# Performance work log

Hardware: AMD Instinct MI355X
Metric: run time of the kernel (lower is better)

## Reference

```python
import jax, jax.numpy as jnp
import numpy as np


def _gen_grid(flow):
    # flow: [N, 2, H, W] -> grid [N, H, W, 2] in normalized [-1,1] coords
    N, _, H, W = flow.shape
    step_y = 2.0 / H
    step_x = 2.0 / W
    gy = jnp.arange(H, dtype=flow.dtype) * step_y + (-1.0 + 0.5 * step_y)
    gx = jnp.arange(W, dtype=flow.dtype) * step_x + (-1.0 + 0.5 * step_x)
    fp = jnp.transpose(flow, (0, 2, 3, 1))  # [N,H,W,2]
    fx = gx[None, None, :] + fp[..., 0]
    fy = gy[None, :, None] + fp[..., 1]
    fx = jnp.remainder(fx + 1.0, 2.0) - 1.0  # wrap x
    return jnp.stack([fx, fy], axis=-1)


def _grid_sample_bilinear(img, grid):
    # img: [N,C,H,W]; grid: [N,H,W,2] normalized, align_corners=False, zero padding
    N, C, H, W = img.shape
    ihwc = jnp.transpose(img, (0, 2, 3, 1))  # [N,H,W,C]
    x = (grid[..., 0] + 1.0) * (W * 0.5) - 0.5
    y = (grid[..., 1] + 1.0) * (H * 0.5) - 0.5
    x0 = jnp.floor(x)
    y0 = jnp.floor(y)
    tx = x - x0
    ty = y - y0
    x0i = x0.astype(jnp.int32)
    y0i = y0.astype(jnp.int32)
    n = jnp.arange(N)[:, None, None]

    def gather(yi, xi):
        valid = (xi >= 0) & (xi < W) & (yi >= 0) & (yi < H)
        v = ihwc[n, jnp.clip(yi, 0, H - 1), jnp.clip(xi, 0, W - 1)]  # [N,H,W,C]
        return v * valid[..., None].astype(img.dtype)

    out = (gather(y0i, x0i) * ((1 - tx) * (1 - ty))[..., None]
           + gather(y0i, x0i + 1) * (tx * (1 - ty))[..., None]
           + gather(y0i + 1, x0i) * ((1 - tx) * ty)[..., None]
           + gather(y0i + 1, x0i + 1) * (tx * ty)[..., None])
    return jnp.transpose(out, (0, 3, 1, 2))  # [N,C,H,W]


def _compose(flow_prev, img_prev, flow_curr, img_curr):
    grid = _gen_grid(flow_curr)
    return (flow_curr + _grid_sample_bilinear(flow_prev, grid),
            img_curr + _grid_sample_bilinear(img_prev, grid))


def setup_inputs() -> dict:
    key = jax.random.key(0)
    k1, k2 = jax.random.split(key)
    B, L, C, H, W = 4, 32, 32, 128, 128
    flows = jax.random.normal(k1, (B, L, 2, H, W), dtype=jnp.float32) * 0.05
    images = jax.random.normal(k2, (B, L, C, H, W), dtype=jnp.float32)
    return {"flows": flows, "images": images}


def reference(flows, images):
    B, L, _, H, W = flows.shape
    C = images.shape[2]
    cf, ci = flows, images
    step = 1
    while step < L:  # static log2(L) iterations
        Lp = L - step
        pf = cf[:, :-step].reshape(B * Lp, 2, H, W)
        pi = ci[:, :-step].reshape(B * Lp, C, H, W)
        qf = cf[:, step:].reshape(B * Lp, 2, H, W)
        qi = ci[:, step:].reshape(B * Lp, C, H, W)
        nf, ni = _compose(pf, pi, qf, qi)
        cf = jnp.concatenate([cf[:, :step], nf.reshape(B, Lp, 2, H, W)], axis=1)
        ci = jnp.concatenate([ci[:, :step], ni.reshape(B, Lp, C, H, W)], axis=1)
        step *= 2
    return ci
```

## Files before the change

kernel.cpp:

```cpp
#include <hip/hip_runtime.h>


constexpr int B_ = 4, L_ = 32, C_ = 32, H_ = 128, W_ = 128;
constexpr int HW = H_ * W_;
constexpr size_t SLICE_I = (size_t)C_ * HW;
constexpr size_t SLICE_F = (size_t)2  * HW;

typedef unsigned short ush;
typedef unsigned int uint;

__device__ __forceinline__ float uasf(uint u){ union{uint i;float f;}v; v.i=u; return v.f; }
__device__ __forceinline__ uint fasu(float f){ union{float f;uint i;}v; v.f=f; return v.i; }
__device__ __forceinline__ uint f2b_u(float f){ uint i=fasu(f); return (i + 0x7FFFu + ((i>>16)&1u))>>16; }

__device__ __forceinline__ void unpack8(const uint4 u, float* f){
    f[0]=uasf(u.x<<16); f[1]=uasf(u.x&0xFFFF0000u);
    f[2]=uasf(u.y<<16); f[3]=uasf(u.y&0xFFFF0000u);
    f[4]=uasf(u.z<<16); f[5]=uasf(u.z&0xFFFF0000u);
    f[6]=uasf(u.w<<16); f[7]=uasf(u.w&0xFFFF0000u);
}
__device__ __forceinline__ uint4 pack8(const float* f){
    uint4 u;
    u.x = f2b_u(f[0]) | (f2b_u(f[1])<<16);
    u.y = f2b_u(f[2]) | (f2b_u(f[3])<<16);
    u.z = f2b_u(f[4]) | (f2b_u(f[5])<<16);
    u.w = f2b_u(f[6]) | (f2b_u(f[7])<<16);
    return u;
}

__device__ __forceinline__ int swz8(int bid, int chunk) {
    return (bid & 7) * chunk + (bid >> 3);
}

struct Samp { float wm00, wm10, wm01, wm11; int q00, q10, q01, q11; };

__device__ __forceinline__ Samp mk(const float2 fc, const int w, const int h)
{
#pragma clang fp contract(off)
    const float step_x = 2.0f / (float)W_;
    const float step_y = 2.0f / (float)H_;
    const float gx = (float)w * step_x + (-1.0f + 0.5f * step_x);
    const float gy = (float)h * step_y + (-1.0f + 0.5f * step_y);
    float fx = gx + fc.x;
    const float fy = gy + fc.y;
    {
        const float tt = fx + 1.0f;
        float r = fmodf(tt, 2.0f);
        if (r < 0.0f) r += 2.0f;
        fx = r - 1.0f;
    }
    const float x = (fx + 1.0f) * ((float)W_ * 0.5f) - 0.5f;
    const float y = (fy + 1.0f) * ((float)H_ * 0.5f) - 0.5f;
    const float x0f = floorf(x), y0f = floorf(y);
    const float tx = x - x0f, ty = y - y0f;
    const int x0 = (int)x0f, y0 = (int)y0f, x1 = x0 + 1, y1 = y0 + 1;
    const float w00 = (1.0f - tx) * (1.0f - ty);
    const float w10 = tx * (1.0f - ty);
    const float w01 = (1.0f - tx) * ty;
    const float w11 = tx * ty;
    const bool vx0 = (x0 >= 0) & (x0 < W_), vx1 = (x1 >= 0) & (x1 < W_);
    const bool vy0 = (y0 >= 0) & (y0 < H_), vy1 = (y1 >= 0) & (y1 < H_);
    const int xc0 = x0 < 0 ? 0 : (x0 >= W_ ? W_ - 1 : x0);
    const int xc1 = x1 < 0 ? 0 : (x1 >= W_ ? W_ - 1 : x1);
    const int yc0 = y0 < 0 ? 0 : (y0 >= H_ ? H_ - 1 : y0);
    const int yc1 = y1 < 0 ? 0 : (y1 >= H_ ? H_ - 1 : y1);
    Samp s;
    s.wm00 = (vy0 & vx0) ? w00 : 0.0f;
    s.wm10 = (vy0 & vx1) ? w10 : 0.0f;
    s.wm01 = (vy1 & vx0) ? w01 : 0.0f;
    s.wm11 = (vy1 & vx1) ? w11 : 0.0f;
    s.q00 = yc0 * W_ + xc0; s.q10 = yc0 * W_ + xc1;
    s.q01 = yc1 * W_ + xc0; s.q11 = yc1 * W_ + xc1;
    return s;
}

__device__ __forceinline__ float2 flowSamp(const float* __restrict__ pF,
                                           const Samp s, const float2 fc)
{
#pragma clang fp contract(off)
    const float2 a = *(const float2*)(pF + (size_t)s.q00 * 2);
    const float2 b = *(const float2*)(pF + (size_t)s.q10 * 2);
    const float2 c = *(const float2*)(pF + (size_t)s.q01 * 2);
    const float2 d = *(const float2*)(pF + (size_t)s.q11 * 2);
    const float sx = ((a.x * s.wm00 + b.x * s.wm10) + c.x * s.wm01) + d.x * s.wm11;
    const float sy = ((a.y * s.wm00 + b.y * s.wm10) + c.y * s.wm01) + d.y * s.wm11;
    return make_float2(fc.x + sx, fc.y + sy);
}

__global__ __launch_bounds__(256)
void prepass_img(const float* __restrict__ src, ush* __restrict__ P,
                 ush* __restrict__ S, float* __restrict__ outN)
{
    constexpr int NB = 32 * 256;
    const int bid = swz8(blockIdx.x, NB / 8);
    const int wc2 = bid & 1, h = (bid >> 1) & 127, l = bid >> 8;
    __shared__ float lds[32][66];
    const int t = threadIdx.x;
    {
        const int c = t >> 3, wq = t & 7;
        const size_t base = (size_t)l * SLICE_I + (size_t)c * HW + h * W_ + wc2 * 64 + wq * 4;
        const float4 v0 = *(const float4*)(src + base);
        const float4 v1 = *(const float4*)(src + base + 32);
        if (l == 0) {
            *(float4*)(outN + base) = v0;
            *(float4*)(outN + base + 32) = v1;
        }
        lds[c][wq*4+0] = v0.x; lds[c][wq*4+1] = v0.y;
        lds[c][wq*4+2] = v0.z; lds[c][wq*4+3] = v0.w;
        lds[c][wq*4+32] = v1.x; lds[c][wq*4+33] = v1.y;
        lds[c][wq*4+34] = v1.z; lds[c][wq*4+35] = v1.w;
    }
    __syncthreads();
    {
        const int pg = t >> 2, lane4 = t & 3;
        float f[8];
        #pragma unroll
        for (int j = 0; j < 8; ++j) f[j] = lds[lane4*8+j][pg];
        ush* dst = (l == 0) ? S : P;
        *(uint4*)(dst + ((size_t)l * HW + h * W_ + wc2 * 64 + pg) * C_ + lane4 * 8) = pack8(f);
    }
}

__global__ __launch_bounds__(256)
void prepass_flow(const float* __restrict__ src, float* __restrict__ F0,
                  float* __restrict__ SF)
{
    constexpr int NB = 32 * HW / 256;
    const int i = swz8(blockIdx.x, NB / 8) * 256 + threadIdx.x;
    const int l = i >> 14;
    const int p = i & (HW - 1);
    const float f0 = src[(size_t)l * SLICE_F + p];
    const float f1 = src[(size_t)l * SLICE_F + HW + p];
    float* dst = (l == 0) ? SF : F0;
    *(float2*)(dst + (size_t)l * SLICE_F + (size_t)p * 2) = make_float2(f0, f1);
}

template<int STEP>
__global__ __launch_bounds__(256)
void compose(const float* __restrict__ Fcur, const ush* __restrict__ Icur,
             float* __restrict__ Fpong, ush* __restrict__ Ipong,
             ush* __restrict__ S, float* __restrict__ SF,
             float* __restrict__ outN)
{
#pragma clang fp contract(off)
    constexpr int NB = (32 - STEP) * 128;
    const int bid = swz8(blockIdx.x, NB / 8);
    const int wc2 = bid & 1, h2 = (bid >> 1) & 63, l = STEP + (bid >> 7);
    const int t = threadIdx.x, lane4 = t & 3, pg = t >> 2;
    const int w = wc2 * 64 + pg;
    const int hA = 2 * h2, hB = hA + 1;
    const int pA = hA * W_ + w, pB = pA + W_;
    const size_t sI = (size_t)l * SLICE_I;
    const size_t sF = (size_t)l * SLICE_F;

    const int prev = l - STEP;
    const ush*   pI = (prev < STEP) ? (S  + (size_t)prev * SLICE_I)
                                    : (Icur + (size_t)prev * SLICE_I);
    const float* pF = (prev < STEP) ? (SF + (size_t)prev * SLICE_F)
                                    : (Fcur + (size_t)prev * SLICE_F);

    const float2 fcA = *(const float2*)(Fcur + sF + (size_t)pA * 2);
    const float2 fcB = *(const float2*)(Fcur + sF + (size_t)pB * 2);
    const Samp sa = mk(fcA, w, hA);
    const Samp sb = mk(fcB, w, hB);

    const uint4 A00 = *(const uint4*)(pI + (size_t)sa.q00 * C_ + lane4 * 8);
    const uint4 A10 = *(const uint4*)(pI + (size_t)sa.q10 * C_ + lane4 * 8);
    const uint4 A01 = *(const uint4*)(pI + (size_t)sa.q01 * C_ + lane4 * 8);
    const uint4 A11 = *(const uint4*)(pI + (size_t)sa.q11 * C_ + lane4 * 8);
    const uint4 B00 = *(const uint4*)(pI + (size_t)sb.q00 * C_ + lane4 * 8);
    const uint4 B10 = *(const uint4*)(pI + (size_t)sb.q10 * C_ + lane4 * 8);
    const uint4 B01 = *(const uint4*)(pI + (size_t)sb.q01 * C_ + lane4 * 8);
    const uint4 B11 = *(const uint4*)(pI + (size_t)sb.q11 * C_ + lane4 * 8);
    const uint4 CA  = *(const uint4*)(Icur + sI + (size_t)pA * C_ + lane4 * 8);
    const uint4 CB  = *(const uint4*)(Icur + sI + (size_t)pB * C_ + lane4 * 8);

    float oA[8], oB[8];
    {
        float g0[8], g1[8], g2[8], g3[8], cu[8];
        unpack8(A00, g0); unpack8(A10, g1); unpack8(A01, g2); unpack8(A11, g3);
        unpack8(CA, cu);
        #pragma unroll
        for (int j = 0; j < 8; ++j) {
            const float s_ = ((g0[j]*sa.wm00 + g1[j]*sa.wm10) + g2[j]*sa.wm01) + g3[j]*sa.wm11;
            oA[j] = cu[j] + s_;
        }
        unpack8(B00, g0); unpack8(B10, g1); unpack8(B01, g2); unpack8(B11, g3);
        unpack8(CB, cu);
        #pragma unroll
        for (int j = 0; j < 8; ++j) {
            const float s_ = ((g0[j]*sb.wm00 + g1[j]*sb.wm10) + g2[j]*sb.wm01) + g3[j]*sb.wm11;
            oB[j] = cu[j] + s_;
        }
    }

    float2 foA, foB;
    const bool doFlow = (lane4 == 0) && (STEP < 16);
    if (doFlow) {
        foA = flowSamp(pF, sa, fcA);
        foB = flowSamp(pF, sb, fcB);
    }

    __shared__ float lds[32][66];
    const bool fin = (STEP == 16) || (l < 2 * STEP);
    if (fin) {
        #pragma unroll
        for (int j = 0; j < 8; ++j) lds[lane4*8+j][pg] = oA[j];
        __syncthreads();
        {
            const int c = t >> 3, wq = t & 7;
            float v[8];
            #pragma unroll
            for (int j2 = 0; j2 < 4; ++j2) {
                const float2 e = *(const float2*)&lds[c][wq*8 + 2*j2];
                v[2*j2] = e.x; v[2*j2+1] = e.y;
            }
            float* dst = outN + sI + (size_t)c * HW + hA * W_ + wc2 * 64 + wq * 8;
            *(float4*)dst       = make_float4(v[0], v[1], v[2], v[3]);
            *(float4*)(dst + 4) = make_float4(v[4], v[5], v[6], v[7]);
        }
        __syncthreads();
        #pragma unroll
        for (int j = 0; j < 8; ++j) lds[lane4*8+j][pg] = oB[j];
        __syncthreads();
        {
            const int c = t >> 3, wq = t & 7;
            float v[8];
            #pragma unroll
            for (int j2 = 0; j2 < 4; ++j2) {
                const float2 e = *(const float2*)&lds[c][wq*8 + 2*j2];
                v[2*j2] = e.x; v[2*j2+1] = e.y;
            }
            float* dst = outN + sI + (size_t)c * HW + hB * W_ + wc2 * 64 + wq * 8;
            *(float4*)dst       = make_float4(v[0], v[1], v[2], v[3]);
            *(float4*)(dst + 4) = make_float4(v[4], v[5], v[6], v[7]);
        }
        if constexpr (STEP < 16) {
            *(uint4*)(S + sI + (size_t)pA * C_ + lane4 * 8) = pack8(oA);
            *(uint4*)(S + sI + (size_t)pB * C_ + lane4 * 8) = pack8(oB);
            if (doFlow) {
                *(float2*)(SF + sF + (size_t)pA * 2) = foA;
                *(float2*)(SF + sF + (size_t)pB * 2) = foB;
            }
        }
    } else {
        *(uint4*)(Ipong + sI + (size_t)pA * C_ + lane4 * 8) = pack8(oA);
        *(uint4*)(Ipong + sI + (size_t)pB * C_ + lane4 * 8) = pack8(oB);
        if (doFlow) {
            *(float2*)(Fpong + sF + (size_t)pA * 2) = foA;
            *(float2*)(Fpong + sF + (size_t)pB * 2) = foB;
        }
    }
}

extern "C" void kernel_launch(void* const* d_in, const int* in_sizes, int n_in,
                              void* d_out, int out_size, void* d_ws, size_t ws_size,
                              hipStream_t stream)
{
    const float* inF = (const float*)d_in[0];
    const float* inI = (const float*)d_in[1];
    float* outI = (float*)d_out;

    char* ws = (char*)d_ws;
    ush*   P  = (ush*)  (ws);
    ush*   Q  = (ush*)  (ws + (size_t)(32 << 20));
    ush*   S  = (ush*)  (ws + (size_t)(64 << 20));
    float* F0 = (float*)(ws + (size_t)(80 << 20));
    float* F1 = (float*)(ws + (size_t)(84 << 20));
    float* SF = (float*)(ws + (size_t)(88 << 20));

    for (int b = 0; b < B_; ++b) {
        const float* bF = inF + (size_t)b * L_ * SLICE_F;
        const float* bI = inI + (size_t)b * L_ * SLICE_I;
        float* bO = outI + (size_t)b * L_ * SLICE_I;

        prepass_img <<<32 * 256, 256, 0, stream>>>(bI, P, S, bO);
        prepass_flow<<<32 * HW / 256, 256, 0, stream>>>(bF, F0, SF);

        compose<1> <<<31 * 128, 256, 0, stream>>>(F0, P, F1, Q, S, SF, bO);
        compose<2> <<<30 * 128, 256, 0, stream>>>(F1, Q, F0, P, S, SF, bO);
        compose<4> <<<28 * 128, 256, 0, stream>>>(F0, P, F1, Q, S, SF, bO);
        compose<8> <<<24 * 128, 256, 0, stream>>>(F1, Q, F0, P, S, SF, bO);
        compose<16><<<16 * 128, 256, 0, stream>>>(F0, P, F1, Q, S, SF, bO);
    }
}
```

Baseline: 847.7 us.

## Process two batches per launch with XCD-aware block-to-slice mapping

Kernels now handle two batch elements per launch instead of one, so the host loop runs twice rather than four times and each launch carries twice the work. Workspace buffers are doubled to hold both batch slots. The block index mapping changes so each XCD owns particular sequence slices (l = lg*8 + xcd), aiming to keep previous and current slices in the same L2. Compose launches a full fixed grid and early-exits blocks with l < STEP, which wastes some block launches in exchange for the regular mapping.

```diff
diff --git a/kernel.cpp b/kernel.cpp
--- a/kernel.cpp
+++ b/kernel.cpp
@@ -91,14 +91,22 @@
 void prepass_img(const float* __restrict__ src, ush* __restrict__ P,
                  ush* __restrict__ S, float* __restrict__ outN)
 {
-    constexpr int NB = 32 * 256;
-    const int bid = swz8(blockIdx.x, NB / 8);
-    const int wc2 = bid & 1, h = (bid >> 1) & 127, l = bid >> 8;
+    const int bid = blockIdx.x;
+    const int xcd = bid & 7;
+    const int r = bid >> 3;
+    const int b = r >> 10;
+    const int r2 = r & 1023;
+    const int lg = r2 >> 8;
+    const int u = r2 & 255;
+    const int l = lg * 8 + xcd;
+    const int h = u >> 1, wc2 = u & 1;
+
     __shared__ float lds[32][66];
     const int t = threadIdx.x;
+    const size_t slotI = (size_t)(b * 32 + l);
     {
         const int c = t >> 3, wq = t & 7;
-        const size_t base = (size_t)l * SLICE_I + (size_t)c * HW + h * W_ + wc2 * 64 + wq * 4;
+        const size_t base = slotI * SLICE_I + (size_t)c * HW + h * W_ + wc2 * 64 + wq * 4;
         const float4 v0 = *(const float4*)(src + base);
         const float4 v1 = *(const float4*)(src + base + 32);
         if (l == 0) {
@@ -116,8 +124,11 @@
         float f[8];
         #pragma unroll
         for (int j = 0; j < 8; ++j) f[j] = lds[lane4*8+j][pg];
-        ush* dst = (l == 0) ? S : P;
-        *(uint4*)(dst + ((size_t)l * HW + h * W_ + wc2 * 64 + pg) * C_ + lane4 * 8) = pack8(f);
+        const size_t pixoff = ((size_t)h * W_ + wc2 * 64 + pg) * C_ + lane4 * 8;
+        if (l == 0)
+            *(uint4*)(S + (size_t)(b * 16) * SLICE_I + pixoff) = pack8(f);
+        else
+            *(uint4*)(P + slotI * SLICE_I + pixoff) = pack8(f);
     }
 }
 
@@ -125,14 +136,17 @@
 void prepass_flow(const float* __restrict__ src, float* __restrict__ F0,
                   float* __restrict__ SF)
 {
-    constexpr int NB = 32 * HW / 256;
+    constexpr int NB = 4096;
     const int i = swz8(blockIdx.x, NB / 8) * 256 + threadIdx.x;
-    const int l = i >> 14;
+    const int la = i >> 14;
+    const int b = la >> 5, l = la & 31;
     const int p = i & (HW - 1);
-    const float f0 = src[(size_t)l * SLICE_F + p];
-    const float f1 = src[(size_t)l * SLICE_F + HW + p];
-    float* dst = (l == 0) ? SF : F0;
-    *(float2*)(dst + (size_t)l * SLICE_F + (size_t)p * 2) = make_float2(f0, f1);
+    const float f0 = src[(size_t)la * SLICE_F + p];
+    const float f1 = src[(size_t)la * SLICE_F + HW + p];
+    if (l == 0)
+        *(float2*)(SF + (size_t)(b * 16) * SLICE_F + (size_t)p * 2) = make_float2(f0, f1);
+    else
+        *(float2*)(F0 + (size_t)la * SLICE_F + (size_t)p * 2) = make_float2(f0, f1);
 }
 
 template<int STEP>
@@ -143,21 +157,30 @@
              float* __restrict__ outN)
 {
 #pragma clang fp contract(off)
-    constexpr int NB = (32 - STEP) * 128;
-    const int bid = swz8(blockIdx.x, NB / 8);
-    const int wc2 = bid & 1, h2 = (bid >> 1) & 63, l = STEP + (bid >> 7);
+    const int bid = blockIdx.x;
+    const int xcd = bid & 7;
+    const int r = bid >> 3;
+    const int b = r >> 9;
+    const int r2 = r & 511;
+    const int lg = r2 >> 7;
+    const int blk = r2 & 127;
+    const int l = lg * 8 + xcd;
+    if (l < STEP) return;
+    const int wc2 = blk & 1, h2 = blk >> 1;
+
     const int t = threadIdx.x, lane4 = t & 3, pg = t >> 2;
     const int w = wc2 * 64 + pg;
     const int hA = 2 * h2, hB = hA + 1;
     const int pA = hA * W_ + w, pB = pA + W_;
-    const size_t sI = (size_t)l * SLICE_I;
-    const size_t sF = (size_t)l * SLICE_F;
+    const size_t slotI = (size_t)(b * 32 + l);
+    const size_t sI = slotI * SLICE_I;
+    const size_t sF = slotI * SLICE_F;
 
     const int prev = l - STEP;
-    const ush*   pI = (prev < STEP) ? (S  + (size_t)prev * SLICE_I)
-                                    : (Icur + (size_t)prev * SLICE_I);
-    const float* pF = (prev < STEP) ? (SF + (size_t)prev * SLICE_F)
-                                    : (Fcur + (size_t)prev * SLICE_F);
+    const ush*   pI = (prev < STEP) ? (S  + (size_t)(b * 16 + prev) * SLICE_I)
+                                    : (Icur + (size_t)(b * 32 + prev) * SLICE_I);
+    const float* pF = (prev < STEP) ? (SF + (size_t)(b * 16 + prev) * SLICE_F)
+                                    : (Fcur + (size_t)(b * 32 + prev) * SLICE_F);
 
     const float2 fcA = *(const float2*)(Fcur + sF + (size_t)pA * 2);
     const float2 fcB = *(const float2*)(Fcur + sF + (size_t)pB * 2);
@@ -236,11 +259,13 @@
             *(float4*)(dst + 4) = make_float4(v[4], v[5], v[6], v[7]);
         }
         if constexpr (STEP < 16) {
-            *(uint4*)(S + sI + (size_t)pA * C_ + lane4 * 8) = pack8(oA);
-            *(uint4*)(S + sI + (size_t)pB * C_ + lane4 * 8) = pack8(oB);
+            const size_t sS = (size_t)(b * 16 + l) * SLICE_I;
+            *(uint4*)(S + sS + (size_t)pA * C_ + lane4 * 8) = pack8(oA);
+            *(uint4*)(S + sS + (size_t)pB * C_ + lane4 * 8) = pack8(oB);
             if (doFlow) {
-                *(float2*)(SF + sF + (size_t)pA * 2) = foA;
-                *(float2*)(SF + sF + (size_t)pB * 2) = foB;
+                const size_t sSF = (size_t)(b * 16 + l) * SLICE_F;
+                *(float2*)(SF + sSF + (size_t)pA * 2) = foA;
+                *(float2*)(SF + sSF + (size_t)pB * 2) = foB;
             }
         }
     } else {
@@ -263,24 +288,24 @@
 
     char* ws = (char*)d_ws;
     ush*   P  = (ush*)  (ws);
-    ush*   Q  = (ush*)  (ws + (size_t)(32 << 20));
-    ush*   S  = (ush*)  (ws + (size_t)(64 << 20));
-    float* F0 = (float*)(ws + (size_t)(80 << 20));
-    float* F1 = (float*)(ws + (size_t)(84 << 20));
-    float* SF = (float*)(ws + (size_t)(88 << 20));
-
-    for (int b = 0; b < B_; ++b) {
-        const float* bF = inF + (size_t)b * L_ * SLICE_F;
-        const float* bI = inI + (size_t)b * L_ * SLICE_I;
-        float* bO = outI + (size_t)b * L_ * SLICE_I;
-
-        prepass_img <<<32 * 256, 256, 0, stream>>>(bI, P, S, bO);
-        prepass_flow<<<32 * HW / 256, 256, 0, stream>>>(bF, F0, SF);
-
-        compose<1> <<<31 * 128, 256, 0, stream>>>(F0, P, F1, Q, S, SF, bO);
-        compose<2> <<<30 * 128, 256, 0, stream>>>(F1, Q, F0, P, S, SF, bO);
-        compose<4> <<<28 * 128, 256, 0, stream>>>(F0, P, F1, Q, S, SF, bO);
-        compose<8> <<<24 * 128, 256, 0, stream>>>(F1, Q, F0, P, S, SF, bO);
-        compose<16><<<16 * 128, 256, 0, stream>>>(F0, P, F1, Q, S, SF, bO);
-    }
-}
+    ush*   Q  = (ush*)  (ws + (size_t)(64  << 20));
+    ush*   S  = (ush*)  (ws + (size_t)(128 << 20));
+    float* F0 = (float*)(ws + (size_t)(160 << 20));
+    float* F1 = (float*)(ws + (size_t)(168 << 20));
+    float* SF = (float*)(ws + (size_t)(176 << 20));
+
+    for (int g = 0; g < 2; ++g) {
+        const float* gF = inF + (size_t)g * 2 * L_ * SLICE_F;
+        const float* gI = inI + (size_t)g * 2 * L_ * SLICE_I;
+        float* gO = outI + (size_t)g * 2 * L_ * SLICE_I;
+
+        prepass_img <<<16384, 256, 0, stream>>>(gI, P, S, gO);
+        prepass_flow<<<4096,  256, 0, stream>>>(gF, F0, SF);
+
+        compose<1> <<<8192, 256, 0, stream>>>(F0, P, F1, Q, S, SF, gO);
+        compose<2> <<<8192, 256, 0, stream>>>(F1, Q, F0, P, S, SF, gO);
+        compose<4> <<<8192, 256, 0, stream>>>(F0, P, F1, Q, S, SF, gO);
+        compose<8> <<<8192, 256, 0, stream>>>(F1, Q, F0, P, S, SF, gO);
+        compose<16><<<8192, 256, 0, stream>>>(F0, P, F1, Q, S, SF, gO);
+    }
+}
```

Result: faster. 774.0 us (-8.7%).
